# Kernel optimization log

Hardware: AMD Instinct MI355X
Metric: run time of the kernel (lower is better)

Reference implementation:

```python
import jax, jax.numpy as jnp
import numpy as np

N_EMBD = 64
N_HEAD = 4
HEAD_DIM = N_EMBD // N_HEAD
EPS = 1e-5


def _layer_norm(x, g, b):
    mu = jnp.mean(x, axis=-1, keepdims=True)
    var = jnp.mean(jnp.square(x - mu), axis=-1, keepdims=True)
    return (x - mu) * jax.lax.rsqrt(var + EPS) * g + b


def setup_inputs() -> dict:
    key = jax.random.key(0)
    ks = jax.random.split(key, 8)
    B, T, C = 4096, 64, N_EMBD
    s = 0.02
    return {
        "x": jax.random.normal(ks[0], (B, T, C), dtype=jnp.float32),
        "ln1_g": jnp.ones((C,), jnp.float32),
        "ln1_b": jnp.zeros((C,), jnp.float32),
        "attn_qkv_w": s * jax.random.normal(ks[1], (C, 3 * C), jnp.float32),
        "attn_qkv_b": jnp.zeros((3 * C,), jnp.float32),
        "attn_proj_w": s * jax.random.normal(ks[2], (C, C), jnp.float32),
        "attn_proj_b": jnp.zeros((C,), jnp.float32),
        "ln2_g": jnp.ones((C,), jnp.float32),
        "ln2_b": jnp.zeros((C,), jnp.float32),
        "fc_w": s * jax.random.normal(ks[3], (C, 4 * C), jnp.float32),
        "fc_b": jnp.zeros((4 * C,), jnp.float32),
        "proj_w": s * jax.random.normal(ks[4], (4 * C, C), jnp.float32),
        "proj_b": jnp.zeros((C,), jnp.float32),
    }


def reference(x, ln1_g, ln1_b, attn_qkv_w, attn_qkv_b, attn_proj_w, attn_proj_b,
              ln2_g, ln2_b, fc_w, fc_b, proj_w, proj_b):
    B, T, C = x.shape
    # --- self-attention branch (dropout in eval mode = identity) ---
    h = _layer_norm(x, ln1_g, ln1_b)
    qkv = h @ attn_qkv_w + attn_qkv_b                      # [B,T,3C]
    q, k, v = jnp.split(qkv, 3, axis=-1)
    def heads(t):
        return t.reshape(B, T, N_HEAD, HEAD_DIM).transpose(0, 2, 1, 3)  # [B,H,T,d]
    q, k, v = heads(q), heads(k), heads(v)
    att = jnp.einsum('bhqd,bhkd->bhqk', q, k) * (1.0 / np.sqrt(HEAD_DIM))
    causal = jnp.tril(jnp.ones((T, T), bool))
    att = jnp.where(causal, att, -jnp.inf)
    att = jax.nn.softmax(att, axis=-1)
    y = jnp.einsum('bhqk,bhkd->bhqd', att, v)              # [B,H,T,d]
    y = y.transpose(0, 2, 1, 3).reshape(B, T, C)
    x = x + (y @ attn_proj_w + attn_proj_b)
    # --- MLP branch ---
    h = _layer_norm(x, ln2_g, ln2_b)
    h = jax.nn.gelu(h @ fc_w + fc_b, approximate=False)
    x = x + (h @ proj_w + proj_b)
    return x
```

## Files before the change

### kernel.cpp

```cpp
#include <hip/hip_runtime.h>
#include <hip/hip_bf16.h>

typedef short bf16x8 __attribute__((ext_vector_type(8)));
typedef short bf16x4 __attribute__((ext_vector_type(4)));
typedef float f32x4  __attribute__((ext_vector_type(4)));
typedef __hip_bfloat16 bf16;

static __device__ __forceinline__ short f2bf(float x) {
    bf16 t = __float2bfloat16(x);
    return *reinterpret_cast<short*>(&t);
}

__global__ void prep_weights(const float* __restrict__ qkv_w,
                             const float* __restrict__ proj_w,
                             const float* __restrict__ fc_w,
                             const float* __restrict__ proj2_w,
                             bf16* __restrict__ ws) {
    int i = blockIdx.x * blockDim.x + threadIdx.x;
    float v;
    if (i < 12288)      { int n = i >> 6,              k = i & 63;    v = qkv_w[k * 192 + n]; }
    else if (i < 16384) { int j = i - 12288, n = j >> 6, k = j & 63;  v = proj_w[k * 64 + n]; }
    else if (i < 32768) { int j = i - 16384, n = j >> 6, k = j & 63;  v = fc_w[k * 256 + n]; }
    else if (i < 49152) { int j = i - 32768, n = j >> 8, k = j & 255; v = proj2_w[k * 64 + n]; }
    else return;
    ws[i] = __float2bfloat16(v);
}

__global__ __launch_bounds__(256, 4)
void gpt_block(const float* __restrict__ x,
               const float* __restrict__ ln1_g, const float* __restrict__ ln1_b,
               const float* __restrict__ qkv_b, const float* __restrict__ proj_b,
               const float* __restrict__ ln2_g, const float* __restrict__ ln2_b,
               const float* __restrict__ fc_b,  const float* __restrict__ proj2_b,
               const bf16* __restrict__ ws,
               float* __restrict__ out) {
    __shared__ __align__(16) char smem[35840];
    bf16* hb = (bf16*)smem;
    bf16* pb = hb;
    bf16* qk = (bf16*)(smem + 9216);
    bf16* vT = (bf16*)(smem + 26624);
    bf16* hm = (bf16*)(smem + 9216);

    const int tid = threadIdx.x;
    const int w   = tid >> 6;
    const int l   = tid & 63;
    const int lr  = l & 15;
    const int lk  = l >> 4;
    const int row = w * 16 + lr;
    const size_t b = blockIdx.x;

    f32x4 xr[4];
    {
        const float* xb = x + b * 4096;
        #pragma unroll
        for (int nt = 0; nt < 4; ++nt)
            xr[nt] = *(const f32x4*)&xb[row * 64 + nt * 16 + lk * 4];
    }

    auto ln = [&](const float* g, const float* be) {
        float s0 = 0.f, s1 = 0.f;
        #pragma unroll
        for (int nt = 0; nt < 4; ++nt)
            #pragma unroll
            for (int r = 0; r < 4; ++r) { float v = xr[nt][r]; s0 += v; s1 += v * v; }
        s0 += __shfl_xor(s0, 16); s1 += __shfl_xor(s1, 16);
        s0 += __shfl_xor(s0, 32); s1 += __shfl_xor(s1, 32);
        float mu   = s0 * (1.f / 64.f);
        float var  = s1 * (1.f / 64.f) - mu * mu;
        float rstd = rsqrtf(var + 1e-5f);
        #pragma unroll
        for (int nt = 0; nt < 4; ++nt) {
            f32x4 g4 = ((const f32x4*)g)[nt * 4 + lk];
            f32x4 b4 = ((const f32x4*)be)[nt * 4 + lk];
            bf16x4 o;
            #pragma unroll
            for (int r = 0; r < 4; ++r)
                o[r] = f2bf((xr[nt][r] - mu) * rstd * g4[r] + b4[r]);
            *(bf16x4*)&hb[row * 72 + nt * 16 + lk * 4] = o;
        }
    };

    ln(ln1_g, ln1_b);
    __syncthreads();

    {
        const short* wsb = (const short*)ws;
        bf16x8 hbf[4][2];
        #pragma unroll
        for (int mt = 0; mt < 4; ++mt)
            #pragma unroll
            for (int ks = 0; ks < 2; ++ks)
                hbf[mt][ks] = *(const bf16x8*)((const short*)hb + (mt * 16 + lr) * 72 + ks * 32 + lk * 8);

        bf16x8 aq[2], ak[2], bv[2];
        #pragma unroll
        for (int ks = 0; ks < 2; ++ks) {
            aq[ks] = *(const bf16x8*)(wsb + (w * 16 + lr) * 64        + ks * 32 + lk * 8);
            ak[ks] = *(const bf16x8*)(wsb + (64 + w * 16 + lr) * 64   + ks * 32 + lk * 8);
            bv[ks] = *(const bf16x8*)(wsb + (128 + w * 16 + lr) * 64  + ks * 32 + lk * 8);
        }
        f32x4 qb = ((const f32x4*)qkv_b)[w * 4 + lk];
        f32x4 kb = ((const f32x4*)qkv_b)[16 + w * 4 + lk];
        float vbias = qkv_b[128 + w * 16 + lr];

        #pragma unroll
        for (int mt = 0; mt < 4; ++mt) {
            f32x4 acc = {};
            #pragma unroll
            for (int ks = 0; ks < 2; ++ks)
                acc = __builtin_amdgcn_mfma_f32_16x16x32_bf16(aq[ks], hbf[mt][ks], acc, 0, 0, 0);
            bf16x4 o;
            #pragma unroll
            for (int r = 0; r < 4; ++r) o[r] = f2bf(acc[r] + qb[r]);
            *(bf16x4*)&qk[(mt * 16 + lr) * 136 + w * 16 + lk * 4] = o;
        }
        #pragma unroll
        for (int mt = 0; mt < 4; ++mt) {
            f32x4 acc = {};
            #pragma unroll
            for (int ks = 0; ks < 2; ++ks)
                acc = __builtin_amdgcn_mfma_f32_16x16x32_bf16(ak[ks], hbf[mt][ks], acc, 0, 0, 0);
            bf16x4 o;
            #pragma unroll
            for (int r = 0; r < 4; ++r) o[r] = f2bf(acc[r] + kb[r]);
            *(bf16x4*)&qk[(mt * 16 + lr) * 136 + 64 + w * 16 + lk * 4] = o;
        }
        #pragma unroll
        for (int mt = 0; mt < 4; ++mt) {
            f32x4 acc = {};
            #pragma unroll
            for (int ks = 0; ks < 2; ++ks)
                acc = __builtin_amdgcn_mfma_f32_16x16x32_bf16(hbf[mt][ks], bv[ks], acc, 0, 0, 0);
            bf16x4 o;
            #pragma unroll
            for (int r = 0; r < 4; ++r) o[r] = f2bf(acc[r] + vbias);
            *(bf16x4*)&vT[(w * 16 + lr) * 72 + mt * 16 + lk * 4] = o;
        }
    }
    __syncthreads();

    {
        bf16x4 z = {};
        for (int kt = w + 1; kt < 4; ++kt)
            *(bf16x4*)&pb[row * 72 + kt * 16 + lk * 4] = z;

        #pragma unroll
        for (int h = 0; h < 4; ++h) {
            bf16x8 qf = {};
            if (lk < 2)
                qf = *(const bf16x8*)((const short*)qk + row * 136 + h * 16 + lk * 8);
            float pr[4][4];
            float psum = 0.f;
            for (int kt = 0; kt <= w; ++kt) {
                bf16x8 kf = {};
                if (lk < 2)
                    kf = *(const bf16x8*)((const short*)qk + (kt * 16 + lr) * 136 + 64 + h * 16 + lk * 8);
                f32x4 acc = {};
                f32x4 sv = __builtin_amdgcn_mfma_f32_16x16x32_bf16(kf, qf, acc, 0, 0, 0);
                #pragma unroll
                for (int r = 0; r < 4; ++r) {
                    float s = sv[r] * 0.25f;
                    if (kt == w && (4 * lk + r) > lr) s = -1e30f;
                    float e = __expf(s);
                    pr[kt][r] = e; psum += e;
                }
            }
            psum += __shfl_xor(psum, 16);
            psum += __shfl_xor(psum, 32);
            float rinv = __builtin_amdgcn_rcpf(psum);
            for (int kt = 0; kt <= w; ++kt) {
                bf16x4 o;
                #pragma unroll
                for (int r = 0; r < 4; ++r) o[r] = f2bf(pr[kt][r] * rinv);
                *(bf16x4*)&pb[row * 72 + kt * 16 + lk * 4] = o;
            }
            f32x4 y = {};
            #pragma unroll
            for (int ks = 0; ks < 2; ++ks) {
                bf16x8 vf = *(const bf16x8*)((const short*)vT + (h * 16 + lr) * 72 + ks * 32 + lk * 8);
                bf16x8 pf = *(const bf16x8*)((const short*)pb + row * 72 + ks * 32 + lk * 8);
                y = __builtin_amdgcn_mfma_f32_16x16x32_bf16(vf, pf, y, 0, 0, 0);
            }
            bf16x4 o;
            #pragma unroll
            for (int r = 0; r < 4; ++r) o[r] = f2bf(y[r]);
            *(bf16x4*)&qk[row * 136 + h * 16 + lk * 4] = o;
        }
    }

    {
        const short* wp = (const short*)ws + 12288;
        bf16x8 yf[2];
        #pragma unroll
        for (int ks = 0; ks < 2; ++ks)
            yf[ks] = *(const bf16x8*)((const short*)qk + row * 136 + ks * 32 + lk * 8);
        #pragma unroll
        for (int nt = 0; nt < 4; ++nt) {
            f32x4 acc = {};
            #pragma unroll
            for (int ks = 0; ks < 2; ++ks) {
                bf16x8 a = *(const bf16x8*)(wp + (nt * 16 + lr) * 64 + ks * 32 + lk * 8);
                acc = __builtin_amdgcn_mfma_f32_16x16x32_bf16(a, yf[ks], acc, 0, 0, 0);
            }
            f32x4 pb4 = ((const f32x4*)proj_b)[nt * 4 + lk];
            #pragma unroll
            for (int r = 0; r < 4; ++r) xr[nt][r] += acc[r] + pb4[r];
        }
    }
    __syncthreads();

    ln(ln2_g, ln2_b);
    __syncthreads();

    f32x4 acc2[4] = {f32x4{}, f32x4{}, f32x4{}, f32x4{}};
    {
        const short* wf = (const short*)ws + 16384;
        const short* w2 = (const short*)ws + 32768;
        for (int H = 0; H < 2; ++H) {
            #pragma unroll
            for (int u = 0; u < 2; ++u) {
                int lt = w + u * 4;
                int gt = H * 8 + lt;
                bf16x8 af[2];
                #pragma unroll
                for (int ks = 0; ks < 2; ++ks)
                    af[ks] = *(const bf16x8*)(wf + (gt * 16 + lr) * 64 + ks * 32 + lk * 8);
                f32x4 fb = ((const f32x4*)fc_b)[gt * 4 + lk];
                #pragma unroll
                for (int mt = 0; mt < 4; ++mt) {
                    f32x4 acc = {};
                    #pragma unroll
                    for (int ks = 0; ks < 2; ++ks) {
                        bf16x8 hf = *(const bf16x8*)((const short*)hb + (mt * 16 + lr) * 72 + ks * 32 + lk * 8);
                        acc = __builtin_amdgcn_mfma_f32_16x16x32_bf16(af[ks], hf, acc, 0, 0, 0);
                    }
                    bf16x4 o;
                    #pragma unroll
                    for (int r = 0; r < 4; ++r) {
                        float v = acc[r] + fb[r];
                        float u_ = v * (0.7978845608f + 0.0356774081f * v * v);
                        u_ = fminf(u_, 8.f);
                        float e = __expf(2.f * u_);
                        float ge = v * e * __builtin_amdgcn_rcpf(1.f + e);
                        o[r] = f2bf(ge);
                    }
                    *(bf16x4*)&hm[(mt * 16 + lr) * 136 + lt * 16 + lk * 4] = o;
                }
            }
            __syncthreads();
            bf16x8 hf4[4];
            #pragma unroll
            for (int ks = 0; ks < 4; ++ks)
                hf4[ks] = *(const bf16x8*)((const short*)hm + row * 136 + ks * 32 + lk * 8);
            #pragma unroll
            for (int nt = 0; nt < 4; ++nt) {
                #pragma unroll
                for (int ks = 0; ks < 4; ++ks) {
                    bf16x8 a = *(const bf16x8*)(w2 + (nt * 16 + lr) * 256 + H * 128 + ks * 32 + lk * 8);
                    acc2[nt] = __builtin_amdgcn_mfma_f32_16x16x32_bf16(a, hf4[ks], acc2[nt], 0, 0, 0);
                }
            }
            if (H == 0) __syncthreads();
        }
    }

    {
        float* ob = out + b * 4096;
        #pragma unroll
        for (int nt = 0; nt < 4; ++nt) {
            f32x4 b2 = ((const f32x4*)proj2_b)[nt * 4 + lk];
            f32x4 o;
            #pragma unroll
            for (int r = 0; r < 4; ++r) o[r] = xr[nt][r] + acc2[nt][r] + b2[r];
            *(f32x4*)&ob[row * 64 + nt * 16 + lk * 4] = o;
        }
    }
}

extern "C" void kernel_launch(void* const* d_in, const int* in_sizes, int n_in,
                              void* d_out, int out_size, void* d_ws, size_t ws_size,
                              hipStream_t stream) {
    const float* x       = (const float*)d_in[0];
    const float* ln1_g   = (const float*)d_in[1];
    const float* ln1_b   = (const float*)d_in[2];
    const float* qkv_w   = (const float*)d_in[3];
    const float* qkv_b   = (const float*)d_in[4];
    const float* proj_w  = (const float*)d_in[5];
    const float* proj_b  = (const float*)d_in[6];
    const float* ln2_g   = (const float*)d_in[7];
    const float* ln2_b   = (const float*)d_in[8];
    const float* fc_w    = (const float*)d_in[9];
    const float* fc_b    = (const float*)d_in[10];
    const float* proj2_w = (const float*)d_in[11];
    const float* proj2_b = (const float*)d_in[12];
    bf16* ws   = (bf16*)d_ws;
    float* out = (float*)d_out;

    prep_weights<<<192, 256, 0, stream>>>(qkv_w, proj_w, fc_w, proj2_w, ws);
    gpt_block<<<4096, 256, 0, stream>>>(x, ln1_g, ln1_b, qkv_b, proj_b,
                                        ln2_g, ln2_b, fc_b, proj2_b, ws, out);
}
```

Before: 244.1 us.

## Make each wave own its rows end-to-end, removing most block barriers

Reorganizes the fused GPT block so each wave computes QKV, attention output projection, LN2 and the MLP for its own 16 rows. Q stays in registers and is redistributed with shuffles, and only K and V^T are shared through LDS. Softmax normalization is deferred to after the PV product, the MLP is chunked per wave with a private LDS scratch, and LDS shrinks so launch bounds can target 5 blocks per CU. This removes most __syncthreads and cross-wave LDS traffic. In exchange every wave now loads the full weight fragments from global/L2 instead of a per-wave slice, and register pressure under the tighter launch bound may cause spills.

Result: slower. 338.7 us (+38.7%).

```diff
diff --git a/kernel.cpp b/kernel.cpp
--- a/kernel.cpp
+++ b/kernel.cpp
@@ -9,6 +9,11 @@
 static __device__ __forceinline__ short f2bf(float x) {
     bf16 t = __float2bfloat16(x);
     return *reinterpret_cast<short*>(&t);
+}
+static __device__ __forceinline__ int pack2(float lo, float hi) {
+    union { short s[2]; int i; } u;
+    u.s[0] = f2bf(lo); u.s[1] = f2bf(hi);
+    return u.i;
 }
 
 __global__ void prep_weights(const float* __restrict__ qkv_w,
@@ -26,7 +31,7 @@
     ws[i] = __float2bfloat16(v);
 }
 
-__global__ __launch_bounds__(256, 4)
+__global__ __launch_bounds__(256, 5)
 void gpt_block(const float* __restrict__ x,
                const float* __restrict__ ln1_g, const float* __restrict__ ln1_b,
                const float* __restrict__ qkv_b, const float* __restrict__ proj_b,
@@ -34,12 +39,9 @@
                const float* __restrict__ fc_b,  const float* __restrict__ proj2_b,
                const bf16* __restrict__ ws,
                float* __restrict__ out) {
-    __shared__ __align__(16) char smem[35840];
-    bf16* hb = (bf16*)smem;
-    bf16* pb = hb;
-    bf16* qk = (bf16*)(smem + 9216);
-    bf16* vT = (bf16*)(smem + 26624);
-    bf16* hm = (bf16*)(smem + 9216);
+    __shared__ __align__(16) char smem[27648];
+    bf16* Kb = (bf16*)(smem + 9216);
+    bf16* vT = (bf16*)(smem + 18432);
 
     const int tid = threadIdx.x;
     const int w   = tid >> 6;
@@ -49,6 +51,10 @@
     const int row = w * 16 + lr;
     const size_t b = blockIdx.x;
 
+    bf16* hbw = (bf16*)smem + w * (16 * 72);
+    bf16* pbw = hbw;
+    bf16* hmw = Kb + w * (16 * 72);
+
     f32x4 xr[4];
     {
         const float* xb = x + b * 4096;
@@ -76,191 +82,184 @@
             #pragma unroll
             for (int r = 0; r < 4; ++r)
                 o[r] = f2bf((xr[nt][r] - mu) * rstd * g4[r] + b4[r]);
-            *(bf16x4*)&hb[row * 72 + nt * 16 + lk * 4] = o;
+            *(bf16x4*)&hbw[lr * 72 + nt * 16 + lk * 4] = o;
         }
     };
 
     ln(ln1_g, ln1_b);
-    __syncthreads();
-
+
+    int qp[8];
     {
         const short* wsb = (const short*)ws;
-        bf16x8 hbf[4][2];
-        #pragma unroll
-        for (int mt = 0; mt < 4; ++mt)
-            #pragma unroll
-            for (int ks = 0; ks < 2; ++ks)
-                hbf[mt][ks] = *(const bf16x8*)((const short*)hb + (mt * 16 + lr) * 72 + ks * 32 + lk * 8);
-
-        bf16x8 aq[2], ak[2], bv[2];
-        #pragma unroll
-        for (int ks = 0; ks < 2; ++ks) {
-            aq[ks] = *(const bf16x8*)(wsb + (w * 16 + lr) * 64        + ks * 32 + lk * 8);
-            ak[ks] = *(const bf16x8*)(wsb + (64 + w * 16 + lr) * 64   + ks * 32 + lk * 8);
-            bv[ks] = *(const bf16x8*)(wsb + (128 + w * 16 + lr) * 64  + ks * 32 + lk * 8);
-        }
-        f32x4 qb = ((const f32x4*)qkv_b)[w * 4 + lk];
-        f32x4 kb = ((const f32x4*)qkv_b)[16 + w * 4 + lk];
-        float vbias = qkv_b[128 + w * 16 + lr];
+        bf16x8 hbf[2];
+        #pragma unroll
+        for (int ks = 0; ks < 2; ++ks)
+            hbf[ks] = *(const bf16x8*)((const short*)hbw + lr * 72 + ks * 32 + lk * 8);
 
         #pragma unroll
         for (int mt = 0; mt < 4; ++mt) {
             f32x4 acc = {};
             #pragma unroll
-            for (int ks = 0; ks < 2; ++ks)
-                acc = __builtin_amdgcn_mfma_f32_16x16x32_bf16(aq[ks], hbf[mt][ks], acc, 0, 0, 0);
-            bf16x4 o;
-            #pragma unroll
-            for (int r = 0; r < 4; ++r) o[r] = f2bf(acc[r] + qb[r]);
-            *(bf16x4*)&qk[(mt * 16 + lr) * 136 + w * 16 + lk * 4] = o;
+            for (int ks = 0; ks < 2; ++ks) {
+                bf16x8 a = *(const bf16x8*)(wsb + (mt * 16 + lr) * 64 + ks * 32 + lk * 8);
+                acc = __builtin_amdgcn_mfma_f32_16x16x32_bf16(a, hbf[ks], acc, 0, 0, 0);
+            }
+            f32x4 qb = ((const f32x4*)qkv_b)[mt * 4 + lk];
+            qp[2 * mt]     = pack2(acc[0] + qb[0], acc[1] + qb[1]);
+            qp[2 * mt + 1] = pack2(acc[2] + qb[2], acc[3] + qb[3]);
         }
         #pragma unroll
         for (int mt = 0; mt < 4; ++mt) {
             f32x4 acc = {};
             #pragma unroll
-            for (int ks = 0; ks < 2; ++ks)
-                acc = __builtin_amdgcn_mfma_f32_16x16x32_bf16(ak[ks], hbf[mt][ks], acc, 0, 0, 0);
+            for (int ks = 0; ks < 2; ++ks) {
+                bf16x8 a = *(const bf16x8*)(wsb + ((64 + mt * 16) + lr) * 64 + ks * 32 + lk * 8);
+                acc = __builtin_amdgcn_mfma_f32_16x16x32_bf16(a, hbf[ks], acc, 0, 0, 0);
+            }
+            f32x4 kb = ((const f32x4*)qkv_b)[16 + mt * 4 + lk];
             bf16x4 o;
             #pragma unroll
             for (int r = 0; r < 4; ++r) o[r] = f2bf(acc[r] + kb[r]);
-            *(bf16x4*)&qk[(mt * 16 + lr) * 136 + 64 + w * 16 + lk * 4] = o;
-        }
-        #pragma unroll
-        for (int mt = 0; mt < 4; ++mt) {
+            *(bf16x4*)&Kb[row * 72 + mt * 16 + lk * 4] = o;
+        }
+        float vbias0 = qkv_b[128 + lr];
+        #pragma unroll
+        for (int nt = 0; nt < 4; ++nt) {
             f32x4 acc = {};
             #pragma unroll
-            for (int ks = 0; ks < 2; ++ks)
-                acc = __builtin_amdgcn_mfma_f32_16x16x32_bf16(hbf[mt][ks], bv[ks], acc, 0, 0, 0);
+            for (int ks = 0; ks < 2; ++ks) {
+                bf16x8 bfr = *(const bf16x8*)(wsb + ((128 + nt * 16) + lr) * 64 + ks * 32 + lk * 8);
+                acc = __builtin_amdgcn_mfma_f32_16x16x32_bf16(hbf[ks], bfr, acc, 0, 0, 0);
+            }
+            float vb = (nt == 0) ? vbias0 : qkv_b[128 + nt * 16 + lr];
             bf16x4 o;
             #pragma unroll
-            for (int r = 0; r < 4; ++r) o[r] = f2bf(acc[r] + vbias);
-            *(bf16x4*)&vT[(w * 16 + lr) * 72 + mt * 16 + lk * 4] = o;
+            for (int r = 0; r < 4; ++r) o[r] = f2bf(acc[r] + vb);
+            *(bf16x4*)&vT[(nt * 16 + lr) * 72 + w * 16 + lk * 4] = o;
         }
     }
     __syncthreads();
 
+    int yp[8];
     {
         bf16x4 z = {};
         for (int kt = w + 1; kt < 4; ++kt)
-            *(bf16x4*)&pb[row * 72 + kt * 16 + lk * 4] = z;
+            *(bf16x4*)&pbw[lr * 72 + kt * 16 + lk * 4] = z;
 
         #pragma unroll
         for (int h = 0; h < 4; ++h) {
-            bf16x8 qf = {};
-            if (lk < 2)
-                qf = *(const bf16x8*)((const short*)qk + row * 136 + h * 16 + lk * 8);
-            float pr[4][4];
+            int c0 = qp[2 * h], c1 = qp[2 * h + 1];
+            int u0 = __shfl_xor(c0, 16), u1 = __shfl_xor(c1, 16);
+            int v0 = __shfl_xor(c0, 32), v1 = __shfl_xor(c1, 32);
+            int w0 = __shfl_xor(v0, 16), w1 = __shfl_xor(v1, 16);
+            bool odd = (lk & 1);
+            union { int i[4]; bf16x8 v; } qu;
+            qu.i[0] = odd ? w0 : c0; qu.i[1] = odd ? w1 : c1;
+            qu.i[2] = odd ? v0 : u0; qu.i[3] = odd ? v1 : u1;
+            bf16x8 qf = qu.v;
+
             float psum = 0.f;
             for (int kt = 0; kt <= w; ++kt) {
                 bf16x8 kf = {};
                 if (lk < 2)
-                    kf = *(const bf16x8*)((const short*)qk + (kt * 16 + lr) * 136 + 64 + h * 16 + lk * 8);
+                    kf = *(const bf16x8*)((const short*)Kb + (kt * 16 + lr) * 72 + h * 16 + lk * 8);
                 f32x4 acc = {};
                 f32x4 sv = __builtin_amdgcn_mfma_f32_16x16x32_bf16(kf, qf, acc, 0, 0, 0);
+                f32x4 e;
                 #pragma unroll
                 for (int r = 0; r < 4; ++r) {
                     float s = sv[r] * 0.25f;
                     if (kt == w && (4 * lk + r) > lr) s = -1e30f;
-                    float e = __expf(s);
-                    pr[kt][r] = e; psum += e;
+                    e[r] = __expf(s);
+                    psum += e[r];
                 }
+                *(bf16x4*)&pbw[lr * 72 + kt * 16 + lk * 4] =
+                    bf16x4{f2bf(e[0]), f2bf(e[1]), f2bf(e[2]), f2bf(e[3])};
             }
             psum += __shfl_xor(psum, 16);
             psum += __shfl_xor(psum, 32);
             float rinv = __builtin_amdgcn_rcpf(psum);
-            for (int kt = 0; kt <= w; ++kt) {
+
+            f32x4 y = {};
+            #pragma unroll
+            for (int ks = 0; ks < 2; ++ks) {
+                bf16x8 vf = *(const bf16x8*)((const short*)vT + (h * 16 + lr) * 72 + ks * 32 + lk * 8);
+                bf16x8 pf = *(const bf16x8*)((const short*)pbw + lr * 72 + ks * 32 + lk * 8);
+                y = __builtin_amdgcn_mfma_f32_16x16x32_bf16(vf, pf, y, 0, 0, 0);
+            }
+            yp[2 * h]     = pack2(y[0] * rinv, y[1] * rinv);
+            yp[2 * h + 1] = pack2(y[2] * rinv, y[3] * rinv);
+        }
+    }
+    __syncthreads();
+
+    {
+        #pragma unroll
+        for (int h = 0; h < 4; ++h) {
+            int2 yv = {yp[2 * h], yp[2 * h + 1]};
+            *(int2*)&pbw[lr * 72 + h * 16 + lk * 4] = yv;
+        }
+        const short* wp = (const short*)ws + 12288;
+        bf16x8 yf[2];
+        #pragma unroll
+        for (int ks = 0; ks < 2; ++ks)
+            yf[ks] = *(const bf16x8*)((const short*)pbw + lr * 72 + ks * 32 + lk * 8);
+        #pragma unroll
+        for (int mt = 0; mt < 4; ++mt) {
+            f32x4 acc = {};
+            #pragma unroll
+            for (int ks = 0; ks < 2; ++ks) {
+                bf16x8 a = *(const bf16x8*)(wp + (mt * 16 + lr) * 64 + ks * 32 + lk * 8);
+                acc = __builtin_amdgcn_mfma_f32_16x16x32_bf16(a, yf[ks], acc, 0, 0, 0);
+            }
+            f32x4 pb4 = ((const f32x4*)proj_b)[mt * 4 + lk];
+            #pragma unroll
+            for (int r = 0; r < 4; ++r) xr[mt][r] += acc[r] + pb4[r];
+        }
+    }
+
+    ln(ln2_g, ln2_b);
+
+    f32x4 acc2[4] = {f32x4{}, f32x4{}, f32x4{}, f32x4{}};
+    {
+        const short* wf = (const short*)ws + 16384;
+        const short* w2 = (const short*)ws + 32768;
+        bf16x8 hbf2[2];
+        #pragma unroll
+        for (int ks = 0; ks < 2; ++ks)
+            hbf2[ks] = *(const bf16x8*)((const short*)hbw + lr * 72 + ks * 32 + lk * 8);
+
+        #pragma unroll
+        for (int c = 0; c < 4; ++c) {
+            #pragma unroll
+            for (int mi = 0; mi < 4; ++mi) {
+                f32x4 acc = {};
+                #pragma unroll
+                for (int ks = 0; ks < 2; ++ks) {
+                    bf16x8 a = *(const bf16x8*)(wf + ((c * 64 + mi * 16) + lr) * 64 + ks * 32 + lk * 8);
+                    acc = __builtin_amdgcn_mfma_f32_16x16x32_bf16(a, hbf2[ks], acc, 0, 0, 0);
+                }
+                f32x4 fb = ((const f32x4*)fc_b)[(c * 4 + mi) * 4 + lk];
                 bf16x4 o;
                 #pragma unroll
-                for (int r = 0; r < 4; ++r) o[r] = f2bf(pr[kt][r] * rinv);
-                *(bf16x4*)&pb[row * 72 + kt * 16 + lk * 4] = o;
-            }
-            f32x4 y = {};
-            #pragma unroll
-            for (int ks = 0; ks < 2; ++ks) {
-                bf16x8 vf = *(const bf16x8*)((const short*)vT + (h * 16 + lr) * 72 + ks * 32 + lk * 8);
-                bf16x8 pf = *(const bf16x8*)((const short*)pb + row * 72 + ks * 32 + lk * 8);
-                y = __builtin_amdgcn_mfma_f32_16x16x32_bf16(vf, pf, y, 0, 0, 0);
-            }
-            bf16x4 o;
-            #pragma unroll
-            for (int r = 0; r < 4; ++r) o[r] = f2bf(y[r]);
-            *(bf16x4*)&qk[row * 136 + h * 16 + lk * 4] = o;
-        }
-    }
-
-    {
-        const short* wp = (const short*)ws + 12288;
-        bf16x8 yf[2];
-        #pragma unroll
-        for (int ks = 0; ks < 2; ++ks)
-            yf[ks] = *(const bf16x8*)((const short*)qk + row * 136 + ks * 32 + lk * 8);
-        #pragma unroll
-        for (int nt = 0; nt < 4; ++nt) {
-            f32x4 acc = {};
-            #pragma unroll
-            for (int ks = 0; ks < 2; ++ks) {
-                bf16x8 a = *(const bf16x8*)(wp + (nt * 16 + lr) * 64 + ks * 32 + lk * 8);
-                acc = __builtin_amdgcn_mfma_f32_16x16x32_bf16(a, yf[ks], acc, 0, 0, 0);
-            }
-            f32x4 pb4 = ((const f32x4*)proj_b)[nt * 4 + lk];
-            #pragma unroll
-            for (int r = 0; r < 4; ++r) xr[nt][r] += acc[r] + pb4[r];
-        }
-    }
-    __syncthreads();
-
-    ln(ln2_g, ln2_b);
-    __syncthreads();
-
-    f32x4 acc2[4] = {f32x4{}, f32x4{}, f32x4{}, f32x4{}};
-    {
-        const short* wf = (const short*)ws + 16384;
-        const short* w2 = (const short*)ws + 32768;
-        for (int H = 0; H < 2; ++H) {
-            #pragma unroll
-            for (int u = 0; u < 2; ++u) {
-                int lt = w + u * 4;
-                int gt = H * 8 + lt;
-                bf16x8 af[2];
+                for (int r = 0; r < 4; ++r) {
+                    float v  = acc[r] + fb[r];
+                    float u_ = v * (0.7978845608f + 0.0356774081f * v * v);
+                    u_ = fminf(u_, 8.f);
+                    float e  = __expf(2.f * u_);
+                    o[r] = f2bf(v * e * __builtin_amdgcn_rcpf(1.f + e));
+                }
+                *(bf16x4*)&hmw[lr * 72 + mi * 16 + lk * 4] = o;
+            }
+            #pragma unroll
+            for (int ks2 = 0; ks2 < 2; ++ks2) {
+                bf16x8 hf = *(const bf16x8*)((const short*)hmw + lr * 72 + ks2 * 32 + lk * 8);
                 #pragma unroll
-                for (int ks = 0; ks < 2; ++ks)
-                    af[ks] = *(const bf16x8*)(wf + (gt * 16 + lr) * 64 + ks * 32 + lk * 8);
-                f32x4 fb = ((const f32x4*)fc_b)[gt * 4 + lk];
-                #pragma unroll
-                for (int mt = 0; mt < 4; ++mt) {
-                    f32x4 acc = {};
-                    #pragma unroll
-                    for (int ks = 0; ks < 2; ++ks) {
-                        bf16x8 hf = *(const bf16x8*)((const short*)hb + (mt * 16 + lr) * 72 + ks * 32 + lk * 8);
-                        acc = __builtin_amdgcn_mfma_f32_16x16x32_bf16(af[ks], hf, acc, 0, 0, 0);
-                    }
-                    bf16x4 o;
-                    #pragma unroll
-                    for (int r = 0; r < 4; ++r) {
-                        float v = acc[r] + fb[r];
-                        float u_ = v * (0.7978845608f + 0.0356774081f * v * v);
-                        u_ = fminf(u_, 8.f);
-                        float e = __expf(2.f * u_);
-                        float ge = v * e * __builtin_amdgcn_rcpf(1.f + e);
-                        o[r] = f2bf(ge);
-                    }
-                    *(bf16x4*)&hm[(mt * 16 + lr) * 136 + lt * 16 + lk * 4] = o;
+                for (int mt2 = 0; mt2 < 4; ++mt2) {
+                    bf16x8 a = *(const bf16x8*)(w2 + (mt2 * 16 + lr) * 256 + c * 64 + ks2 * 32 + lk * 8);
+                    acc2[mt2] = __builtin_amdgcn_mfma_f32_16x16x32_bf16(a, hf, acc2[mt2], 0, 0, 0);
                 }
             }
-            __syncthreads();
-            bf16x8 hf4[4];
-            #pragma unroll
-            for (int ks = 0; ks < 4; ++ks)
-                hf4[ks] = *(const bf16x8*)((const short*)hm + row * 136 + ks * 32 + lk * 8);
-            #pragma unroll
-            for (int nt = 0; nt < 4; ++nt) {
-                #pragma unroll
-                for (int ks = 0; ks < 4; ++ks) {
-                    bf16x8 a = *(const bf16x8*)(w2 + (nt * 16 + lr) * 256 + H * 128 + ks * 32 + lk * 8);
-                    acc2[nt] = __builtin_amdgcn_mfma_f32_16x16x32_bf16(a, hf4[ks], acc2[nt], 0, 0, 0);
-                }
-            }
-            if (H == 0) __syncthreads();
         }
     }
 
```
